# Kernel tuning notes

Hardware: AMD Instinct MI355X
Metric: run time of the kernel (lower is better)

## Reference

```python
import jax, jax.numpy as jnp
import numpy as np

BETA = 0.5

def setup_inputs() -> dict:
    key = jax.random.key(0)
    ks = jax.random.split(key, 10)
    B, H = 4096, 200
    ITEM, REGION = 100000, 1000
    D, HID = 128, 64  # embed_size, hidden_size
    half = D // 2
    history = jax.random.randint(ks[0], (B, H), 0, ITEM)
    target = jax.random.randint(ks[1], (B,), 0, ITEM)
    history_region = jax.random.randint(ks[2], (B, H), 0, REGION)
    target_region = jax.random.randint(ks[3], (B,), 0, REGION)
    W_hist = jax.random.normal(ks[4], (ITEM, half), jnp.float32) * 0.01
    W_tgt = jax.random.normal(ks[5], (ITEM, half), jnp.float32) * 0.01
    W_reg = jax.random.normal(ks[6], (REGION, half), jnp.float32) * 0.01
    W1 = jax.random.normal(ks[7], (D, HID), jnp.float32) * (1.0 / np.sqrt(D))
    b1 = jnp.zeros((HID,), jnp.float32)
    W2 = jax.random.normal(ks[8], (HID,), jnp.float32) * (1.0 / np.sqrt(HID))
    return {"history": history, "target": target,
            "history_region": history_region, "target_region": target_region,
            "W_hist": W_hist, "W_tgt": W_tgt, "W_reg": W_reg,
            "W1": W1, "b1": b1, "W2": W2}

def reference(history, target, history_region, target_region,
              W_hist, W_tgt, W_reg, W1, b1, W2):
    # gather + concat: [B,H,D] and [B,D]
    h = jnp.concatenate([W_hist[history], W_reg[history_region]], axis=-1)
    t = jnp.concatenate([W_tgt[target], W_reg[target_region]], axis=-1)
    inp = h * t[:, None, :]                      # [B,H,D]
    r1 = jax.nn.relu(inp @ W1 + b1)              # [B,H,HID] (dropout = identity at eval)
    logits = r1 @ W2                             # [B,H]
    mask = (history != target[:, None]).astype(logits.dtype)
    exp_A = jnp.exp(logits) * mask               # [B,H]
    exp_sum = jnp.sum(exp_A, axis=-1) ** BETA    # [B], beta-power normalization
    attn = exp_A / exp_sum[:, None]              # [B,H]
    pred = jnp.einsum('bhd,bd->b', h * attn[..., None], t)
    return jax.nn.sigmoid(pred)
```

## Files before the change

kernel.cpp:

```cpp
#include <hip/hip_runtime.h>
#include <math.h>

#define NB        4096
#define NH        200
#define HIST_ROWS 100000
#define REG_ROWS  1000
#define NTILES    13

typedef __attribute__((ext_vector_type(4))) int   int4i;

#define SA 2048.0f
#define SB 16384.0f
#define ST 2048.0f
#define INV_LOGIT (1.0f / (SA * SB))
#define INV_S     (1.0f / (SA * ST))

__device__ __forceinline__ int q8(float x, float s) {
    return __float2int_rn(fminf(fmaxf(x * s, -127.f), 127.f));
}
__device__ __forceinline__ int pack4(float a, float b, float c, float d, float s) {
    const int x0 = q8(a, s), x1 = q8(b, s), x2 = q8(c, s), x3 = q8(d, s);
    return (x0 & 255) | ((x1 & 255) << 8) | ((x2 & 255) << 16) | (x3 << 24);
}

__global__ __launch_bounds__(256) void prep_i8(
    const float* __restrict__ Wh, const float* __restrict__ Wr,
    const float* __restrict__ W1,
    unsigned char* __restrict__ tab, float* __restrict__ W1F2)
{
    const int total = (HIST_ROWS + REG_ROWS) * 16;
    const int HE    = HIST_ROWS * 16;
    unsigned* dst = (unsigned*)tab;
    for (int i = blockIdx.x * blockDim.x + threadIdx.x; i < total;
         i += gridDim.x * blockDim.x) {
        const float4 v = (i < HE) ? ((const float4*)Wh)[i]
                                  : ((const float4*)Wr)[i - HE];
        dst[i] = (unsigned)pack4(v.x, v.y, v.z, v.w, SA);
    }
    if (blockIdx.x == 0) {
        for (int i = threadIdx.x; i < 10240; i += 256) {
            const int chunk = i >> 4, j = i & 15;
            const int frag = chunk >> 6, nt = frag >> 1, ks = frag & 1;
            const int c = chunk & 63, q = c >> 4, l = c & 15;
            W1F2[i] = (nt < 4) ? W1[(ks * 64 + q * 16 + j) * 64 + nt * 16 + l] : 0.f;
        }
    }
}

__device__ __forceinline__ void epi_store_i8(
    const int4i* accT, const float* w2v, const float* b1v,
    int tl, int quad, int l15, float* logit_lds, float* s_lds)
{
    float part[4] = {0.f, 0.f, 0.f, 0.f};
    #pragma unroll
    for (int nt = 0; nt < 4; ++nt)
        #pragma unroll
        for (int r = 0; r < 4; ++r)
            part[r] += fmaxf((float)accT[nt][r] * INV_LOGIT + b1v[nt], 0.f) * w2v[nt];
    #pragma unroll
    for (int r = 0; r < 4; ++r) {
        part[r] += __shfl_xor(part[r], 1);
        part[r] += __shfl_xor(part[r], 2);
        part[r] += __shfl_xor(part[r], 4);
        part[r] += __shfl_xor(part[r], 8);
    }
    if (l15 == 0) {
        const int jg = tl * 16 + quad * 4;
        #pragma unroll
        for (int r = 0; r < 4; ++r) {
            logit_lds[jg + r] = part[r];
            s_lds[jg + r]     = (float)accT[4][r] * INV_S;
        }
    }
}

__device__ __forceinline__ int4i quant_row_fp32(const float* row, int quad) {
    const float4* p = (const float4*)(row + quad * 16);
    const float4 v0 = p[0], v1 = p[1], v2 = p[2], v3 = p[3];
    int4i o;
    o.x = pack4(v0.x, v0.y, v0.z, v0.w, SA);
    o.y = pack4(v1.x, v1.y, v1.z, v1.w, SA);
    o.z = pack4(v2.x, v2.y, v2.z, v2.w, SA);
    o.w = pack4(v3.x, v3.y, v3.z, v3.w, SA);
    return o;
}

template <bool BT>
__global__ __launch_bounds__(256, 3) void nais_i8(
    const int*   __restrict__ history,
    const int*   __restrict__ target,
    const int*   __restrict__ history_region,
    const int*   __restrict__ target_region,
    const float* __restrict__ W_hist,
    const float* __restrict__ W_tgt,
    const float* __restrict__ W_reg,
    const float* __restrict__ W1,
    const float* __restrict__ b1,
    const float* __restrict__ W2,
    const unsigned char* __restrict__ tab,
    const float* __restrict__ W1F2,
    float*       __restrict__ out)
{
    __shared__ int hist_lds[224];
    __shared__ int hreg_lds[224];
    __shared__ __align__(16) float t_lds[128];
    __shared__ __align__(16) int Bf4[640 * 4];
    __shared__ float logit_lds[208];
    __shared__ float s_lds[208];
    __shared__ float red_e[4], red_p[4];

    const int b   = blockIdx.x;
    const int tid = threadIdx.x;
    const int tgt = target[b];

    if (tid < 224) {
        const int jj = tid < NH ? tid : NH - 1;
        hist_lds[tid] = history[b * NH + jj];
        hreg_lds[tid] = history_region[b * NH + jj];
    }
    if (tid < 64) {
        t_lds[tid] = W_tgt[(size_t)tgt * 64 + tid];
    } else if (tid < 128) {
        t_lds[tid] = W_reg[(size_t)target_region[b] * 64 + (tid - 64)];
    }
    __syncthreads();

    const int lane = tid & 63, wv = tid >> 6;
    const int l15  = lane & 15, quad = lane >> 4;

    const int  tls[4] = {wv, wv + 4, wv + 8, wv + 12};
    const bool has3   = (tls[3] < NTILES);

    int4i A[4][2];
    if (BT) {
        #pragma unroll
        for (int tt = 0; tt < 4; ++tt) {
            const int j  = ((tt == 3 && !has3) ? tls[2] : tls[tt]) * 16 + l15;
            const int ih = hist_lds[j], ir = hreg_lds[j];
            A[tt][0] = *(const int4i*)(tab + (size_t)ih * 64 + quad * 16);
            A[tt][1] = *(const int4i*)(tab + (size_t)(HIST_ROWS + ir) * 64 + quad * 16);
        }
    }

    #pragma unroll
    for (int v = 0; v < 3; ++v) {
        const int i = tid + v * 256;
        if (i < 640) {
            const int frag = i >> 6, nt = frag >> 1, ks = frag & 1;
            const int c = i & 63, q = c >> 4, l = c & 15;
            const int k0 = ks * 64 + q * 16;
            const float4 t0 = *(const float4*)(t_lds + k0);
            const float4 t1 = *(const float4*)(t_lds + k0 + 4);
            const float4 t2 = *(const float4*)(t_lds + k0 + 8);
            const float4 t3 = *(const float4*)(t_lds + k0 + 12);
            int4i ob;
            if (nt < 4) {
                float4 w0, w1, w2, w3;
                if (BT) {
                    const float4* wp = (const float4*)(W1F2 + i * 16);
                    w0 = wp[0]; w1 = wp[1]; w2 = wp[2]; w3 = wp[3];
                } else {
                    const int n = nt * 16 + l;
                    float tmp[16];
                    #pragma unroll
                    for (int j = 0; j < 16; ++j) tmp[j] = W1[(k0 + j) * 64 + n];
                    w0 = make_float4(tmp[0], tmp[1], tmp[2], tmp[3]);
                    w1 = make_float4(tmp[4], tmp[5], tmp[6], tmp[7]);
                    w2 = make_float4(tmp[8], tmp[9], tmp[10], tmp[11]);
                    w3 = make_float4(tmp[12], tmp[13], tmp[14], tmp[15]);
                }
                ob.x = pack4(w0.x * t0.x, w0.y * t0.y, w0.z * t0.z, w0.w * t0.w, SB);
                ob.y = pack4(w1.x * t1.x, w1.y * t1.y, w1.z * t1.z, w1.w * t1.w, SB);
                ob.z = pack4(w2.x * t2.x, w2.y * t2.y, w2.z * t2.z, w2.w * t2.w, SB);
                ob.w = pack4(w3.x * t3.x, w3.y * t3.y, w3.z * t3.z, w3.w * t3.w, SB);
            } else {
                if (l == 0) {
                    ob.x = pack4(t0.x, t0.y, t0.z, t0.w, ST);
                    ob.y = pack4(t1.x, t1.y, t1.z, t1.w, ST);
                    ob.z = pack4(t2.x, t2.y, t2.z, t2.w, ST);
                    ob.w = pack4(t3.x, t3.y, t3.z, t3.w, ST);
                } else {
                    ob = (int4i){0, 0, 0, 0};
                }
            }
            *reinterpret_cast<int4i*>(&Bf4[i * 4]) = ob;
        }
    }
    __syncthreads();

    float w2v[4], b1v[4];
    #pragma unroll
    for (int nt = 0; nt < 4; ++nt) {
        w2v[nt] = W2[nt * 16 + l15];
        b1v[nt] = b1[nt * 16 + l15];
    }

    #pragma unroll
    for (int pp = 0; pp < 2; ++pp) {
        const int t0i = pp * 2, t1i = pp * 2 + 1;
        const bool hb = (t1i < 3) || has3;

        if (!BT) {
            #pragma unroll
            for (int tt = 0; tt < 2; ++tt) {
                const int ti = t0i + tt;
                const int j  = ((ti == 3 && !has3) ? tls[2] : tls[ti]) * 16 + l15;
                A[ti][0] = quant_row_fp32(W_hist + (size_t)hist_lds[j] * 64, quad);
                A[ti][1] = quant_row_fp32(W_reg  + (size_t)hreg_lds[j] * 64, quad);
            }
        }

        int4i acc[2][5];
        #pragma unroll
        for (int tt = 0; tt < 2; ++tt)
            #pragma unroll
            for (int nt = 0; nt < 5; ++nt) acc[tt][nt] = (int4i){0, 0, 0, 0};

        #pragma unroll
        for (int ks = 0; ks < 2; ++ks) {
            int4i bf[5];
            #pragma unroll
            for (int nt = 0; nt < 5; ++nt)
                bf[nt] = *reinterpret_cast<const int4i*>(&Bf4[((nt * 2 + ks) * 64 + lane) * 4]);
            #pragma unroll
            for (int nt = 0; nt < 5; ++nt)
                acc[0][nt] = __builtin_amdgcn_mfma_i32_16x16x64_i8(A[t0i][ks], bf[nt], acc[0][nt], 0, 0, 0);
            if (hb) {
                #pragma unroll
                for (int nt = 0; nt < 5; ++nt)
                    acc[1][nt] = __builtin_amdgcn_mfma_i32_16x16x64_i8(A[t1i][ks], bf[nt], acc[1][nt], 0, 0, 0);
            }
        }

        epi_store_i8(acc[0], w2v, b1v, tls[t0i], quad, l15, logit_lds, s_lds);
        if (hb) epi_store_i8(acc[1], w2v, b1v, tls[t1i], quad, l15, logit_lds, s_lds);
    }
    __syncthreads();

    float e = 0.f, p = 0.f;
    if (tid < NH) {
        const float ex = (hist_lds[tid] != tgt) ? expf(logit_lds[tid]) : 0.f;
        e = ex;
        p = ex * s_lds[tid];
    }
    #pragma unroll
    for (int off = 32; off > 0; off >>= 1) {
        e += __shfl_down(e, off);
        p += __shfl_down(p, off);
    }
    if (lane == 0) { red_e[wv] = e; red_p[wv] = p; }
    __syncthreads();
    if (tid == 0) {
        const float E = red_e[0] + red_e[1] + red_e[2] + red_e[3];
        const float P = red_p[0] + red_p[1] + red_p[2] + red_p[3];
        const float pred = P / sqrtf(E);
        out[b] = 1.f / (1.f + expf(-pred));
    }
}

extern "C" void kernel_launch(void* const* d_in, const int* in_sizes, int n_in,
                              void* d_out, int out_size, void* d_ws, size_t ws_size,
                              hipStream_t stream) {
    const int*   history        = (const int*)  d_in[0];
    const int*   target         = (const int*)  d_in[1];
    const int*   history_region = (const int*)  d_in[2];
    const int*   target_region  = (const int*)  d_in[3];
    const float* W_hist         = (const float*)d_in[4];
    const float* W_tgt          = (const float*)d_in[5];
    const float* W_reg          = (const float*)d_in[6];
    const float* W1             = (const float*)d_in[7];
    const float* b1             = (const float*)d_in[8];
    const float* W2             = (const float*)d_in[9];
    float* out = (float*)d_out;

    const size_t tab_bytes = (size_t)(HIST_ROWS + REG_ROWS) * 64;
    const size_t need = tab_bytes + 10240 * 4;
    if (ws_size >= need) {
        unsigned char* tab = (unsigned char*)d_ws;
        float* W1F2 = (float*)((char*)d_ws + tab_bytes);
        prep_i8<<<2048, 256, 0, stream>>>(W_hist, W_reg, W1, tab, W1F2);
        nais_i8<true><<<NB, 256, 0, stream>>>(history, target, history_region, target_region,
                                              W_hist, W_tgt, W_reg, W1, b1, W2, tab, W1F2, out);
    } else {
        nais_i8<false><<<NB, 256, 0, stream>>>(history, target, history_region, target_region,
                                               W_hist, W_tgt, W_reg, W1, b1, W2, nullptr, nullptr, out);
    }
}
```

Before: 144.6 us.

## Precompute per-batch int8 B fragments in prep kernel and drop LDS staging

Moves construction of the per-sample quantized (W1*t) and t fragments from the main kernel into the prep kernel, which now runs extra blocks per batch row and writes them to a 40 MB workspace buffer. The main kernel loads these fragments straight into registers and reads history indices directly from global memory, removing the LDS setup phase and two block barriers. The aim is a shorter main-kernel prologue. The cost is a large extra global write and read of the fragment buffer, plus a bigger prep kernel.

```diff
diff --git a/kernel.cpp b/kernel.cpp
--- a/kernel.cpp
+++ b/kernel.cpp
@@ -7,7 +7,7 @@
 #define REG_ROWS  1000
 #define NTILES    13
 
-typedef __attribute__((ext_vector_type(4))) int   int4i;
+typedef __attribute__((ext_vector_type(4))) int int4i;
 
 #define SA 2048.0f
 #define SB 16384.0f
@@ -23,26 +23,60 @@
     return (x0 & 255) | ((x1 & 255) << 8) | ((x2 & 255) << 16) | (x3 << 24);
 }
 
-__global__ __launch_bounds__(256) void prep_i8(
+__global__ __launch_bounds__(256) void prep_all(
+    const int*   __restrict__ target,
+    const int*   __restrict__ target_region,
     const float* __restrict__ Wh, const float* __restrict__ Wr,
-    const float* __restrict__ W1,
-    unsigned char* __restrict__ tab, float* __restrict__ W1F2)
+    const float* __restrict__ Wt, const float* __restrict__ W1,
+    unsigned char* __restrict__ tab, signed char* __restrict__ Ball)
 {
-    const int total = (HIST_ROWS + REG_ROWS) * 16;
-    const int HE    = HIST_ROWS * 16;
-    unsigned* dst = (unsigned*)tab;
-    for (int i = blockIdx.x * blockDim.x + threadIdx.x; i < total;
-         i += gridDim.x * blockDim.x) {
-        const float4 v = (i < HE) ? ((const float4*)Wh)[i]
-                                  : ((const float4*)Wr)[i - HE];
-        dst[i] = (unsigned)pack4(v.x, v.y, v.z, v.w, SA);
-    }
-    if (blockIdx.x == 0) {
-        for (int i = threadIdx.x; i < 10240; i += 256) {
-            const int chunk = i >> 4, j = i & 15;
-            const int frag = chunk >> 6, nt = frag >> 1, ks = frag & 1;
-            const int c = chunk & 63, q = c >> 4, l = c & 15;
-            W1F2[i] = (nt < 4) ? W1[(ks * 64 + q * 16 + j) * 64 + nt * 16 + l] : 0.f;
+    if (blockIdx.x < NB) {
+        const int b    = blockIdx.x;
+        const int tgt  = target[b];
+        const int treg = target_region[b];
+        #pragma unroll
+        for (int v = 0; v < 3; ++v) {
+            const int i = threadIdx.x + v * 256;
+            if (i < 640) {
+                const int frag = i >> 6, nt = frag >> 1, ks = frag & 1;
+                const int c = i & 63, q = c >> 4, l = c & 15;
+                const float* tp = ks ? (Wr + (size_t)treg * 64) : (Wt + (size_t)tgt * 64);
+                const float4 t0 = *(const float4*)(tp + q * 16);
+                const float4 t1 = *(const float4*)(tp + q * 16 + 4);
+                const float4 t2 = *(const float4*)(tp + q * 16 + 8);
+                const float4 t3 = *(const float4*)(tp + q * 16 + 12);
+                int4i ob;
+                if (nt < 4) {
+                    const int n = nt * 16 + l;
+                    float w[16];
+                    #pragma unroll
+                    for (int j = 0; j < 16; ++j)
+                        w[j] = W1[(ks * 64 + q * 16 + j) * 64 + n];
+                    ob.x = pack4(w[0]*t0.x,  w[1]*t0.y,  w[2]*t0.z,  w[3]*t0.w,  SB);
+                    ob.y = pack4(w[4]*t1.x,  w[5]*t1.y,  w[6]*t1.z,  w[7]*t1.w,  SB);
+                    ob.z = pack4(w[8]*t2.x,  w[9]*t2.y,  w[10]*t2.z, w[11]*t2.w, SB);
+                    ob.w = pack4(w[12]*t3.x, w[13]*t3.y, w[14]*t3.z, w[15]*t3.w, SB);
+                } else {
+                    if (l == 0) {
+                        ob.x = pack4(t0.x, t0.y, t0.z, t0.w, ST);
+                        ob.y = pack4(t1.x, t1.y, t1.z, t1.w, ST);
+                        ob.z = pack4(t2.x, t2.y, t2.z, t2.w, ST);
+                        ob.w = pack4(t3.x, t3.y, t3.z, t3.w, ST);
+                    } else {
+                        ob = (int4i){0, 0, 0, 0};
+                    }
+                }
+                *reinterpret_cast<int4i*>(Ball + ((size_t)b * 640 + i) * 16) = ob;
+            }
+        }
+    } else {
+        const int total = (HIST_ROWS + REG_ROWS) * 16;
+        const int HE    = HIST_ROWS * 16;
+        unsigned* dst = (unsigned*)tab;
+        for (int i = (blockIdx.x - NB) * 256 + threadIdx.x; i < total; i += 2048 * 256) {
+            const float4 v = (i < HE) ? ((const float4*)Wh)[i]
+                                      : ((const float4*)Wr)[i - HE];
+            dst[i] = (unsigned)pack4(v.x, v.y, v.z, v.w, SA);
         }
     }
 }
@@ -71,6 +105,104 @@
             logit_lds[jg + r] = part[r];
             s_lds[jg + r]     = (float)accT[4][r] * INV_S;
         }
+    }
+}
+
+__global__ __launch_bounds__(256, 3) void nais_i8s(
+    const int*   __restrict__ history,
+    const int*   __restrict__ target,
+    const int*   __restrict__ history_region,
+    const float* __restrict__ b1,
+    const float* __restrict__ W2,
+    const unsigned char* __restrict__ tab,
+    const signed char*   __restrict__ Ball,
+    float*       __restrict__ out)
+{
+    __shared__ float logit_lds[208];
+    __shared__ float s_lds[208];
+    __shared__ float red_e[4], red_p[4];
+
+    const int b   = blockIdx.x;
+    const int tid = threadIdx.x;
+    const int lane = tid & 63, wv = tid >> 6;
+    const int l15  = lane & 15, quad = lane >> 4;
+    const int tgt  = target[b];
+
+    const int  tls[4] = {wv, wv + 4, wv + 8, wv + 12};
+    const bool has3   = (tls[3] < NTILES);
+
+    int4i A[4][2];
+    #pragma unroll
+    for (int tt = 0; tt < 4; ++tt) {
+        int j = ((tt == 3 && !has3) ? tls[2] : tls[tt]) * 16 + l15;
+        j = j < NH ? j : NH - 1;
+        const int ih = history[b * NH + j];
+        const int ir = history_region[b * NH + j];
+        A[tt][0] = *(const int4i*)(tab + (size_t)ih * 64 + quad * 16);
+        A[tt][1] = *(const int4i*)(tab + (size_t)(HIST_ROWS + ir) * 64 + quad * 16);
+    }
+
+    int4i BF[10];
+    const int4i* bp = (const int4i*)(Ball + (size_t)b * 640 * 16);
+    #pragma unroll
+    for (int f = 0; f < 10; ++f) BF[f] = bp[f * 64 + lane];
+
+    float w2v[4], b1v[4];
+    #pragma unroll
+    for (int nt = 0; nt < 4; ++nt) {
+        w2v[nt] = W2[nt * 16 + l15];
+        b1v[nt] = b1[nt * 16 + l15];
+    }
+
+    #pragma unroll
+    for (int pp = 0; pp < 2; ++pp) {
+        const int  t0i = pp * 2, t1i = pp * 2 + 1;
+        const bool hb  = (pp == 0) || has3;
+
+        int4i acc[2][5];
+        #pragma unroll
+        for (int tt = 0; tt < 2; ++tt)
+            #pragma unroll
+            for (int nt = 0; nt < 5; ++nt) acc[tt][nt] = (int4i){0, 0, 0, 0};
+
+        #pragma unroll
+        for (int ks = 0; ks < 2; ++ks) {
+            #pragma unroll
+            for (int nt = 0; nt < 5; ++nt)
+                acc[0][nt] = __builtin_amdgcn_mfma_i32_16x16x64_i8(
+                    A[t0i][ks], BF[nt * 2 + ks], acc[0][nt], 0, 0, 0);
+            if (hb) {
+                #pragma unroll
+                for (int nt = 0; nt < 5; ++nt)
+                    acc[1][nt] = __builtin_amdgcn_mfma_i32_16x16x64_i8(
+                        A[t1i][ks], BF[nt * 2 + ks], acc[1][nt], 0, 0, 0);
+            }
+        }
+
+        epi_store_i8(acc[0], w2v, b1v, tls[t0i], quad, l15, logit_lds, s_lds);
+        if (hb) epi_store_i8(acc[1], w2v, b1v, tls[t1i], quad, l15, logit_lds, s_lds);
+    }
+    __syncthreads();
+
+    float e = 0.f, p = 0.f;
+    if (tid < NH) {
+        const int hj = history[b * NH + tid];
+        const float ex = (hj != tgt) ? expf(logit_lds[tid]) : 0.f;
+        e = ex;
+        p = ex * s_lds[tid];
+    }
+    #pragma unroll
+    for (int off = 32; off > 0; off >>= 1) {
+        e += __shfl_down(e, off);
+        p += __shfl_down(p, off);
+    }
+    if (lane == 0) { red_e[wv] = e; red_p[wv] = p; }
+    __syncthreads();
+    if (tid == 0) {
+        const float E = red_e[0] + red_e[1] + red_e[2] + red_e[3];
+        const float P = red_p[0] + red_p[1] + red_p[2] + red_p[3];
+        const float pred = P / sqrtf(E);
+        out[b] = 1.f / (1.f + expf(-pred));
     }
 }
 
@@ -85,8 +217,7 @@
     return o;
 }
 
-template <bool BT>
-__global__ __launch_bounds__(256, 3) void nais_i8(
+__global__ __launch_bounds__(256, 3) void nais_i8_fb(
     const int*   __restrict__ history,
     const int*   __restrict__ target,
     const int*   __restrict__ history_region,
@@ -97,8 +228,6 @@
     const float* __restrict__ W1,
     const float* __restrict__ b1,
     const float* __restrict__ W2,
-    const unsigned char* __restrict__ tab,
-    const float* __restrict__ W1F2,
     float*       __restrict__ out)
 {
     __shared__ int hist_lds[224];
@@ -127,20 +256,8 @@
 
     const int lane = tid & 63, wv = tid >> 6;
     const int l15  = lane & 15, quad = lane >> 4;
-
     const int  tls[4] = {wv, wv + 4, wv + 8, wv + 12};
     const bool has3   = (tls[3] < NTILES);
-
-    int4i A[4][2];
-    if (BT) {
-        #pragma unroll
-        for (int tt = 0; tt < 4; ++tt) {
-            const int j  = ((tt == 3 && !has3) ? tls[2] : tls[tt]) * 16 + l15;
-            const int ih = hist_lds[j], ir = hreg_lds[j];
-            A[tt][0] = *(const int4i*)(tab + (size_t)ih * 64 + quad * 16);
-            A[tt][1] = *(const int4i*)(tab + (size_t)(HIST_ROWS + ir) * 64 + quad * 16);
-        }
-    }
 
     #pragma unroll
     for (int v = 0; v < 3; ++v) {
@@ -155,24 +272,14 @@
             const float4 t3 = *(const float4*)(t_lds + k0 + 12);
             int4i ob;
             if (nt < 4) {
-                float4 w0, w1, w2, w3;
-                if (BT) {
-                    const float4* wp = (const float4*)(W1F2 + i * 16);
-                    w0 = wp[0]; w1 = wp[1]; w2 = wp[2]; w3 = wp[3];
-                } else {
-                    const int n = nt * 16 + l;
-                    float tmp[16];
-                    #pragma unroll
-                    for (int j = 0; j < 16; ++j) tmp[j] = W1[(k0 + j) * 64 + n];
-                    w0 = make_float4(tmp[0], tmp[1], tmp[2], tmp[3]);
-                    w1 = make_float4(tmp[4], tmp[5], tmp[6], tmp[7]);
-                    w2 = make_float4(tmp[8], tmp[9], tmp[10], tmp[11]);
-                    w3 = make_float4(tmp[12], tmp[13], tmp[14], tmp[15]);
-                }
-                ob.x = pack4(w0.x * t0.x, w0.y * t0.y, w0.z * t0.z, w0.w * t0.w, SB);
-                ob.y = pack4(w1.x * t1.x, w1.y * t1.y, w1.z * t1.z, w1.w * t1.w, SB);
-                ob.z = pack4(w2.x * t2.x, w2.y * t2.y, w2.z * t2.z, w2.w * t2.w, SB);
-                ob.w = pack4(w3.x * t3.x, w3.y * t3.y, w3.z * t3.z, w3.w * t3.w, SB);
+                const int n = nt * 16 + l;
+                float w[16];
+                #pragma unroll
+                for (int j = 0; j < 16; ++j) w[j] = W1[(k0 + j) * 64 + n];
+                ob.x = pack4(w[0]*t0.x,  w[1]*t0.y,  w[2]*t0.z,  w[3]*t0.w,  SB);
+                ob.y = pack4(w[4]*t1.x,  w[5]*t1.y,  w[6]*t1.z,  w[7]*t1.w,  SB);
+                ob.z = pack4(w[8]*t2.x,  w[9]*t2.y,  w[10]*t2.z, w[11]*t2.w, SB);
+                ob.w = pack4(w[12]*t3.x, w[13]*t3.y, w[14]*t3.z, w[15]*t3.w, SB);
             } else {
                 if (l == 0) {
                     ob.x = pack4(t0.x, t0.y, t0.z, t0.w, ST);
@@ -197,17 +304,16 @@
 
     #pragma unroll
     for (int pp = 0; pp < 2; ++pp) {
-        const int t0i = pp * 2, t1i = pp * 2 + 1;
-        const bool hb = (t1i < 3) || has3;
-
-        if (!BT) {
-            #pragma unroll
-            for (int tt = 0; tt < 2; ++tt) {
-                const int ti = t0i + tt;
-                const int j  = ((ti == 3 && !has3) ? tls[2] : tls[ti]) * 16 + l15;
-                A[ti][0] = quant_row_fp32(W_hist + (size_t)hist_lds[j] * 64, quad);
-                A[ti][1] = quant_row_fp32(W_reg  + (size_t)hreg_lds[j] * 64, quad);
-            }
+        const int  t0i = pp * 2, t1i = pp * 2 + 1;
+        const bool hb  = (pp == 0) || has3;
+
+        int4i A[2][2];
+        #pragma unroll
+        for (int tt = 0; tt < 2; ++tt) {
+            const int ti = t0i + tt;
+            const int j  = ((ti == 3 && !has3) ? tls[2] : tls[ti]) * 16 + l15;
+            A[tt][0] = quant_row_fp32(W_hist + (size_t)hist_lds[j] * 64, quad);
+            A[tt][1] = quant_row_fp32(W_reg  + (size_t)hreg_lds[j] * 64, quad);
         }
 
         int4i acc[2][5];
@@ -224,11 +330,11 @@
                 bf[nt] = *reinterpret_cast<const int4i*>(&Bf4[((nt * 2 + ks) * 64 + lane) * 4]);
             #pragma unroll
             for (int nt = 0; nt < 5; ++nt)
-                acc[0][nt] = __builtin_amdgcn_mfma_i32_16x16x64_i8(A[t0i][ks], bf[nt], acc[0][nt], 0, 0, 0);
+                acc[0][nt] = __builtin_amdgcn_mfma_i32_16x16x64_i8(A[0][ks], bf[nt], acc[0][nt], 0, 0, 0);
             if (hb) {
                 #pragma unroll
                 for (int nt = 0; nt < 5; ++nt)
-                    acc[1][nt] = __builtin_amdgcn_mfma_i32_16x16x64_i8(A[t1i][ks], bf[nt], acc[1][nt], 0, 0, 0);
+                    acc[1][nt] = __builtin_amdgcn_mfma_i32_16x16x64_i8(A[1][ks], bf[nt], acc[1][nt], 0, 0, 0);
             }
         }
 
@@ -273,16 +379,17 @@
     const float* W2             = (const float*)d_in[9];
     float* out = (float*)d_out;
 
-    const size_t tab_bytes = (size_t)(HIST_ROWS + REG_ROWS) * 64;
-    const size_t need = tab_bytes + 10240 * 4;
-    if (ws_size >= need) {
-        unsigned char* tab = (unsigned char*)d_ws;
-        float* W1F2 = (float*)((char*)d_ws + tab_bytes);
-        prep_i8<<<2048, 256, 0, stream>>>(W_hist, W_reg, W1, tab, W1F2);
-        nais_i8<true><<<NB, 256, 0, stream>>>(history, target, history_region, target_region,
-                                              W_hist, W_tgt, W_reg, W1, b1, W2, tab, W1F2, out);
+    const size_t tab_bytes  = (size_t)(HIST_ROWS + REG_ROWS) * 64;
+    const size_t ball_bytes = (size_t)NB * 640 * 16;
+    if (ws_size >= tab_bytes + ball_bytes) {
+        unsigned char* tab  = (unsigned char*)d_ws;
+        signed char*   Ball = (signed char*)d_ws + tab_bytes;
+        prep_all<<<NB + 2048, 256, 0, stream>>>(target, target_region,
+                                                W_hist, W_reg, W_tgt, W1, tab, Ball);
+        nais_i8s<<<NB, 256, 0, stream>>>(history, target, history_region,
+                                         b1, W2, tab, Ball, out);
     } else {
-        nais_i8<false><<<NB, 256, 0, stream>>>(history, target, history_region, target_region,
-                                               W_hist, W_tgt, W_reg, W1, b1, W2, nullptr, nullptr, out);
-    }
-}
+        nais_i8_fb<<<NB, 256, 0, stream>>>(history, target, history_region, target_region,
+                                           W_hist, W_tgt, W_reg, W1, b1, W2, out);
+    }
+}
```

Result: slower. 148.1 us (+2.4%).
